# Optimization experiments

Measured on AMD Instinct MI355X. Metric: run time of the kernel, lower is better.

Reference implementation:

```python
import jax, jax.numpy as jnp
import numpy as np

N = 100000      # nodes
E = 1600000     # edges (avg in-degree 16)
IN_DIM = 256
HID_DIM = 256
OUT_DIM = 32
K = 16          # propagation hops


def _xavier(key, fan_in, fan_out, gain=1.0):
    a = gain * (6.0 / (fan_in + fan_out)) ** 0.5
    return jax.random.uniform(key, (fan_in, fan_out), jnp.float32, -a, a)


def setup_inputs() -> dict:
    key = jax.random.key(0)
    ks = jax.random.split(key, 8)
    feats = jax.random.normal(ks[0], (N, IN_DIM), jnp.float32)
    relu_gain = 2.0 ** 0.5
    W1 = _xavier(ks[1], IN_DIM, HID_DIM, relu_gain)
    b1 = jnp.zeros((HID_DIM,), jnp.float32)
    W2 = _xavier(ks[2], HID_DIM, HID_DIM, relu_gain)
    b2 = jnp.zeros((HID_DIM,), jnp.float32)
    W3 = _xavier(ks[3], HID_DIM, OUT_DIM, 1.0)
    b3 = jnp.zeros((OUT_DIM,), jnp.float32)
    s = _xavier(ks[4], OUT_DIM, 1, 1.0)  # sigmoid gain = 1.0
    src = jax.random.randint(ks[5], (E,), 0, N, jnp.int32)
    dst = jax.random.randint(ks[6], (E,), 0, N, jnp.int32)
    return {"feats": feats, "W1": W1, "b1": b1, "W2": W2, "b2": b2,
            "W3": W3, "b3": b3, "s": s, "src": src, "dst": dst}


def reference(feats, W1, b1, W2, b2, W3, b3, s, src, dst):
    # MLP stack (dropout is identity at inference)
    x = jax.nn.relu(feats @ W1 + b1)
    x = jax.nn.relu(x @ W2 + b2)
    x = x @ W3 + b3  # [N, OUT_DIM]

    # symmetric degree normalization from in-degrees (count of dst)
    degs = jax.ops.segment_sum(jnp.ones((E,), jnp.float32), dst, num_segments=N)
    norm = jnp.where(degs > 0, degs ** -0.5, 0.0)[:, None]  # [N,1]

    # k-hop normalized SpMM propagation: h <- D^-1/2 A^T D^-1/2 h
    def step(h, _):
        msgs = (h * norm)[src]                                  # gather, [E,D]
        h2 = jax.ops.segment_sum(msgs, dst, num_segments=N) * norm
        return h2, h2

    _, hs = jax.lax.scan(step, x, None, length=K)  # [K, N, D]
    H = jnp.concatenate([x[None], hs], axis=0).transpose(1, 0, 2)  # [N, K+1, D]

    # sigmoid-gated attention pooling over hops
    S = jax.nn.sigmoid(jnp.einsum('nkd,d->nk', H, s[:, 0]))  # [N, K+1]
    out = jnp.einsum('nk,nkd->nd', S, H)                      # [N, D]
    return out
```

## Files before the change

### kernel.cpp

```cpp
#include <hip/hip_runtime.h>
#include <hip/hip_bf16.h>
#include <cstdint>

typedef short bf16x8 __attribute__((ext_vector_type(8)));
typedef float f32x4 __attribute__((ext_vector_type(4)));
typedef unsigned short u16x8 __attribute__((ext_vector_type(8)));

#define BSHIFT 8
#define NBMAX 512

__device__ __forceinline__ ushort f2bf(float x) {
  uint32_t u = __float_as_uint(x);
  u += 0x7FFFu + ((u >> 16) & 1u);
  return (ushort)(u >> 16);
}
__device__ __forceinline__ float bf2f(ushort b) {
  return __uint_as_float((uint32_t)b << 16);
}

__device__ __forceinline__ void gload16(const void* g, void* l) {
  __builtin_amdgcn_global_load_lds((const __attribute__((address_space(1))) uint32_t*)g,
                                   (__attribute__((address_space(3))) uint32_t*)l, 16, 0, 0);
}

__global__ __launch_bounds__(256) void k_f32_to_bf16(const float* __restrict__ in,
                                                     ushort* __restrict__ out, int n4) {
  int i = blockIdx.x * 256 + threadIdx.x;
  if (i >= n4) return;
  const float4 v = reinterpret_cast<const float4*>(in)[i];
  ushort4 o;
  o.x = f2bf(v.x); o.y = f2bf(v.y); o.z = f2bf(v.z); o.w = f2bf(v.w);
  reinterpret_cast<ushort4*>(out)[i] = o;
}

__global__ __launch_bounds__(256) void k_convT(const float* __restrict__ W,
                                               ushort* __restrict__ Bt, int K, int Nc) {
  int i = blockIdx.x * 256 + threadIdx.x;
  if (i >= K * Nc) return;
  int nn = i / K, kk = i - nn * K;
  Bt[i] = f2bf(W[kk * Nc + nn]);
}

__global__ __launch_bounds__(256) void k_gemm1(const ushort* __restrict__ A,
                                               const ushort* __restrict__ Bt,
                                               const float* __restrict__ bias,
                                               ushort* __restrict__ Cout, int M, int ldc) {
  constexpr int BM = 128, BK = 64, KTOT = 256;
  constexpr int WM = 64, WN = 64, MR = 4, NR = 4;
  __shared__ ushort lA[2][BM * BK];
  __shared__ ushort lB[2][BM * BK];
  const int tid = threadIdx.x;
  const int w = tid >> 6, lane = tid & 63;
  const int wr = w >> 1, wc = w & 1;
  const int bm = blockIdx.x * BM;
  const int bn = blockIdx.y * BM;
  f32x4 acc[MR][NR] = {};

  auto stage = [&](int buf, int ks) {
    #pragma unroll
    for (int c0 = 0; c0 < 4; ++c0) {
      int c = c0 * 256 + tid;
      int r = c >> 3, ch = c & 7;
      int sch = (ch ^ (r & 7)) << 3;
      gload16(A + (size_t)(bm + r) * KTOT + ks + sch, lA[buf] + c * 8);
      gload16(Bt + (size_t)(bn + r) * KTOT + ks + sch, lB[buf] + c * 8);
    }
  };

  stage(0, 0);
  __syncthreads();
  int cur = 0;
  for (int kst = 0; kst < 4; ++kst) {
    if (kst < 3) stage(cur ^ 1, (kst + 1) * BK);
    #pragma unroll
    for (int kk = 0; kk < 2; ++kk) {
      bf16x8 af[MR], bfr[NR];
      int kc = kk * 4 + (lane >> 4);
      #pragma unroll
      for (int m = 0; m < MR; ++m) {
        int r = wr * WM + m * 16 + (lane & 15);
        af[m] = *reinterpret_cast<const bf16x8*>(lA[cur] + r * BK + (kc ^ (r & 7)) * 8);
      }
      #pragma unroll
      for (int n = 0; n < NR; ++n) {
        int r = wc * WN + n * 16 + (lane & 15);
        bfr[n] = *reinterpret_cast<const bf16x8*>(lB[cur] + r * BK + (kc ^ (r & 7)) * 8);
      }
      #pragma unroll
      for (int m = 0; m < MR; ++m)
        #pragma unroll
        for (int n = 0; n < NR; ++n)
          acc[m][n] = __builtin_amdgcn_mfma_f32_16x16x32_bf16(af[m], bfr[n], acc[m][n], 0, 0, 0);
    }
    __syncthreads();
    cur ^= 1;
  }
  #pragma unroll
  for (int m = 0; m < MR; ++m) {
    #pragma unroll
    for (int n = 0; n < NR; ++n) {
      int col = bn + wc * WN + n * 16 + (lane & 15);
      float bv = bias[col];
      #pragma unroll
      for (int j = 0; j < 4; ++j) {
        int row = bm + wr * WM + m * 16 + (lane >> 4) * 4 + j;
        if (row < M) {
          float v = fmaxf(acc[m][n][j] + bv, 0.f);
          Cout[(size_t)row * ldc + col] = f2bf(v);
        }
      }
    }
  }
}

__global__ __launch_bounds__(256) void k_gemm23(const ushort* __restrict__ x1,
                                                const ushort* __restrict__ w2t,
                                                const float* __restrict__ b2,
                                                const ushort* __restrict__ w3t,
                                                const float* __restrict__ b3,
                                                const float* __restrict__ svec,
                                                const float* __restrict__ nrm,
                                                float* __restrict__ xout,
                                                ushort* __restrict__ hs0, int M) {
  constexpr int BM = 64, BK = 64, KTOT = 256;
  constexpr int MR = 4, NR = 4;
  __shared__ char smem[40960];
  ushort* lA = (ushort*)smem;
  ushort* lB = (ushort*)(smem + 8192);
  ushort* lh2 = (ushort*)smem;
  const int tid = threadIdx.x;
  const int wv = tid >> 6, lane = tid & 63;
  const int bm = blockIdx.x * BM;
  f32x4 acc[MR][NR] = {};

  for (int ks = 0; ks < KTOT; ks += BK) {
    #pragma unroll
    for (int c0 = 0; c0 < 2; ++c0) {
      int c = c0 * 256 + tid;
      int r = c >> 3, ch = c & 7;
      gload16(x1 + (size_t)(bm + r) * KTOT + ks + ((ch ^ (r & 7)) << 3), lA + c * 8);
    }
    #pragma unroll
    for (int c0 = 0; c0 < 8; ++c0) {
      int c = c0 * 256 + tid;
      int r = c >> 3, ch = c & 7;
      gload16(w2t + (size_t)r * KTOT + ks + ((ch ^ (r & 7)) << 3), lB + c * 8);
    }
    __syncthreads();
    #pragma unroll
    for (int kk = 0; kk < 2; ++kk) {
      bf16x8 af[MR], bfr[NR];
      int kc = kk * 4 + (lane >> 4);
      #pragma unroll
      for (int m = 0; m < MR; ++m) {
        int r = m * 16 + (lane & 15);
        af[m] = *reinterpret_cast<const bf16x8*>(lA + r * BK + (kc ^ (r & 7)) * 8);
      }
      #pragma unroll
      for (int n = 0; n < NR; ++n) {
        int r = wv * 64 + n * 16 + (lane & 15);
        bfr[n] = *reinterpret_cast<const bf16x8*>(lB + r * BK + (kc ^ (r & 7)) * 8);
      }
      #pragma unroll
      for (int m = 0; m < MR; ++m)
        #pragma unroll
        for (int n = 0; n < NR; ++n)
          acc[m][n] = __builtin_amdgcn_mfma_f32_16x16x32_bf16(af[m], bfr[n], acc[m][n], 0, 0, 0);
    }
    __syncthreads();
  }

  #pragma unroll
  for (int n = 0; n < NR; ++n) {
    int col = wv * 64 + n * 16 + (lane & 15);
    float bv = b2[col];
    #pragma unroll
    for (int m = 0; m < MR; ++m) {
      #pragma unroll
      for (int j = 0; j < 4; ++j) {
        int row = m * 16 + (lane >> 4) * 4 + j;
        float v = fmaxf(acc[m][n][j] + bv, 0.f);
        int ch = col >> 3;
        int within = col & 7;
        lh2[row * 256 + ((ch ^ (row & 7)) << 3) + within] = f2bf(v);
      }
    }
  }
  __syncthreads();

  f32x4 acc3[2] = {};
  #pragma unroll
  for (int ks3 = 0; ks3 < 8; ++ks3) {
    int row = wv * 16 + (lane & 15);
    int kc = ks3 * 4 + (lane >> 4);
    bf16x8 af = *reinterpret_cast<const bf16x8*>(lh2 + row * 256 + ((kc ^ (row & 7)) << 3));
    #pragma unroll
    for (int n = 0; n < 2; ++n) {
      int col = n * 16 + (lane & 15);
      bf16x8 bfr = *reinterpret_cast<const bf16x8*>(w3t + (size_t)col * KTOT + kc * 8);
      acc3[n] = __builtin_amdgcn_mfma_f32_16x16x32_bf16(af, bfr, acc3[n], 0, 0, 0);
    }
  }
  float bb0 = b3[(lane & 15)];
  float bb1 = b3[16 + (lane & 15)];
  float sv0 = svec[(lane & 15)];
  float sv1 = svec[16 + (lane & 15)];
  #pragma unroll
  for (int j = 0; j < 4; ++j) {
    float x0 = acc3[0][j] + bb0;
    float x1v = acc3[1][j] + bb1;
    float p = x0 * sv0 + x1v * sv1;
    #pragma unroll
    for (int msk = 1; msk <= 8; msk <<= 1) p += __shfl_xor(p, msk);
    float g = 1.f / (1.f + __expf(-p));
    int row = bm + wv * 16 + (lane >> 4) * 4 + j;
    if (row < M) {
      float nv = nrm[row];
      xout[(size_t)row * 32 + (lane & 15)] = g * x0;
      xout[(size_t)row * 32 + 16 + (lane & 15)] = g * x1v;
      hs0[(size_t)row * 32 + (lane & 15)] = f2bf(x0 * nv);
      hs0[(size_t)row * 32 + 16 + (lane & 15)] = f2bf(x1v * nv);
    }
  }
}

__global__ __launch_bounds__(256) void k_bucket_hist(const int* __restrict__ dst,
                                                     int* __restrict__ bhist, int E) {
  __shared__ int lh[NBMAX];
  const int t = threadIdx.x;
  const int base = blockIdx.x * 4096;
  for (int i = t; i < NBMAX; i += 256) lh[i] = 0;
  __syncthreads();
  #pragma unroll
  for (int j = 0; j < 16; ++j) {
    int e = base + t + j * 256;
    if (e < E) atomicAdd(&lh[dst[e] >> BSHIFT], 1);
  }
  __syncthreads();
  for (int i = t; i < NBMAX; i += 256)
    if (lh[i]) atomicAdd(&bhist[i], lh[i]);
}

__global__ __launch_bounds__(256) void k_bucket_scan(const int* __restrict__ bhist,
                                                     int* __restrict__ bbase) {
  __shared__ int sh[256];
  int t = threadIdx.x;
  int v0 = bhist[2 * t], v1 = bhist[2 * t + 1];
  int s = v0 + v1;
  sh[t] = s;
  __syncthreads();
  for (int off = 1; off < 256; off <<= 1) {
    int x = (t >= off) ? sh[t - off] : 0;
    __syncthreads();
    sh[t] += x;
    __syncthreads();
  }
  int pre = sh[t] - s;
  bbase[2 * t] = pre;
  bbase[2 * t + 1] = pre + v0;
  if (t == 255) bbase[NBMAX] = sh[255];
}

__global__ __launch_bounds__(256) void k_bucket_scatter(const int* __restrict__ src,
                                                        const int* __restrict__ dst,
                                                        const int* __restrict__ bbase,
                                                        int* __restrict__ gfill,
                                                        int* __restrict__ tmp,
                                                        int E, int nbuck) {
  __shared__ int lhist[NBMAX];
  __shared__ int lbase[NBMAX];
  const int t = threadIdx.x;
  const int base = blockIdx.x * 4096;
  for (int i = t; i < NBMAX; i += 256) lhist[i] = 0;
  __syncthreads();
  int myd[16];
  #pragma unroll
  for (int j = 0; j < 16; ++j) {
    int e = base + t + j * 256;
    myd[j] = (e < E) ? dst[e] : -1;
    if (myd[j] >= 0) atomicAdd(&lhist[myd[j] >> BSHIFT], 1);
  }
  __syncthreads();
  for (int i = t; i < nbuck; i += 256) {
    int c = lhist[i];
    lbase[i] = (c > 0) ? atomicAdd(&gfill[i], c) : 0;
    lhist[i] = 0;
  }
  __syncthreads();
  #pragma unroll
  for (int j = 0; j < 16; ++j) {
    int e = base + t + j * 256;
    if (myd[j] >= 0) {
      int b = myd[j] >> BSHIFT;
      int r = atomicAdd(&lhist[b], 1);
      int pos = bbase[b] + lbase[b] + r;
      tmp[pos] = src[e] | ((myd[j] & 255) << 17);
    }
  }
}

__global__ __launch_bounds__(256) void k_bucket_sort(const int* __restrict__ tmp,
                                                     const int* __restrict__ bbase,
                                                     int* __restrict__ rp,
                                                     float* __restrict__ nrm,
                                                     float* __restrict__ invdeg,
                                                     float* __restrict__ sdeg,
                                                     int* __restrict__ ss,
                                                     int Nn, int E) {
  __shared__ int lcnt[256];
  __shared__ int sh[256];
  __shared__ int lpre[256];
  __shared__ int lfill[256];
  const int t = threadIdx.x;
  const int b = blockIdx.x;
  const int node0 = b << BSHIFT;
  const int seg0 = bbase[b], seg1 = bbase[b + 1];
  lcnt[t] = 0;
  lfill[t] = 0;
  __syncthreads();
  for (int i = seg0 + t; i < seg1; i += 256)
    atomicAdd(&lcnt[tmp[i] >> 17], 1);
  __syncthreads();
  int c = lcnt[t];
  sh[t] = c;
  __syncthreads();
  for (int off = 1; off < 256; off <<= 1) {
    int x = (t >= off) ? sh[t - off] : 0;
    __syncthreads();
    sh[t] += x;
    __syncthreads();
  }
  int pre = seg0 + sh[t] - c;
  lpre[t] = pre;
  int node = node0 + t;
  if (node < Nn) {
    rp[node] = pre;
    nrm[node] = (c > 0) ? rsqrtf((float)c) : 0.f;
    invdeg[node] = (c > 0) ? (1.f / (float)c) : 0.f;
    sdeg[node] = sqrtf((float)c);
  }
  if (b == 0 && t == 0) rp[Nn] = E;
  __syncthreads();
  for (int i = seg0 + t; i < seg1; i += 256) {
    int p = tmp[i];
    int n = p >> 17;
    int r = atomicAdd(&lfill[n], 1);
    ss[lpre[n] + r] = p & 0x1FFFF;
  }
}

__global__ __launch_bounds__(256) void k_prop(const ushort* __restrict__ hs_in,
                                              ushort* __restrict__ hs_out,
                                              const int* __restrict__ rp,
                                              const int* __restrict__ ss,
                                              const float* __restrict__ invdeg, int Nn) {
  const int wave = threadIdx.x >> 6;
  const int lane = threadIdx.x & 63;
  const int e4 = lane >> 4;
  const int d16 = lane & 15;
  const int v = blockIdx.x * 4 + wave;
  if (v >= Nn) return;
  const int beg = rp[v], end = rp[v + 1];
  float a0 = 0.f, a1 = 0.f;
  if (beg < end) {
    const int last = end - 1;
    const int i0 = beg + e4, i1 = i0 + 4, i2 = i0 + 8, i3 = i0 + 12;
    const int u0 = ss[min(i0, last)];
    const int u1 = ss[min(i1, last)];
    const int u2 = ss[min(i2, last)];
    const int u3 = ss[min(i3, last)];
    const uint r0 = *reinterpret_cast<const uint*>(hs_in + (size_t)u0 * 32 + d16 * 2);
    const uint r1 = *reinterpret_cast<const uint*>(hs_in + (size_t)u1 * 32 + d16 * 2);
    const uint r2 = *reinterpret_cast<const uint*>(hs_in + (size_t)u2 * 32 + d16 * 2);
    const uint r3 = *reinterpret_cast<const uint*>(hs_in + (size_t)u3 * 32 + d16 * 2);
    const float m0 = (i0 < end) ? 1.f : 0.f;
    const float m1 = (i1 < end) ? 1.f : 0.f;
    const float m2 = (i2 < end) ? 1.f : 0.f;
    const float m3 = (i3 < end) ? 1.f : 0.f;
    a0 = m0 * bf2f((ushort)r0) + m1 * bf2f((ushort)r1)
       + m2 * bf2f((ushort)r2) + m3 * bf2f((ushort)r3);
    a1 = m0 * bf2f((ushort)(r0 >> 16)) + m1 * bf2f((ushort)(r1 >> 16))
       + m2 * bf2f((ushort)(r2 >> 16)) + m3 * bf2f((ushort)(r3 >> 16));
    for (int i = i0 + 16; i < end; i += 4) {
      int u = ss[i];
      uint r = *reinterpret_cast<const uint*>(hs_in + (size_t)u * 32 + d16 * 2);
      a0 += bf2f((ushort)r);
      a1 += bf2f((ushort)(r >> 16));
    }
  }
  a0 += __shfl_xor(a0, 16); a1 += __shfl_xor(a1, 16);
  a0 += __shfl_xor(a0, 32); a1 += __shfl_xor(a1, 32);
  if (e4 == 0) {
    const float idv = invdeg[v];
    uint o = (uint)f2bf(a0 * idv) | ((uint)f2bf(a1 * idv) << 16);
    *reinterpret_cast<uint*>(hs_out + (size_t)v * 32 + d16 * 2) = o;
  }
}

__global__ __launch_bounds__(256) void k_pool(const ushort* __restrict__ hsF,
                                              const ushort* __restrict__ hsX,
                                              const ushort* __restrict__ hs16,
                                              const float* __restrict__ sdeg,
                                              const float* __restrict__ svec,
                                              float* __restrict__ xout, int Nn) {
  const int t = blockIdx.x * 256 + threadIdx.x;
  const int v = t >> 2;
  const int d4 = t & 3;
  if (v >= Nn) return;
  const float sd = sdeg[v];
  const float4 svA = *reinterpret_cast<const float4*>(svec + d4 * 8);
  const float4 svB = *reinterpret_cast<const float4*>(svec + d4 * 8 + 4);
  const size_t seg = (size_t)Nn * 32;
  const size_t off = (size_t)v * 32 + d4 * 8;
  float o0 = 0, o1 = 0, o2 = 0, o3 = 0, o4 = 0, o5 = 0, o6 = 0, o7 = 0;
  #pragma unroll
  for (int k = 1; k <= 16; ++k) {
    const ushort* hp = (k < 8) ? (hsF + (size_t)k * seg)
                     : (k < 16) ? (hsX + (size_t)(k - 8) * seg)
                                : hs16;
    u16x8 h = *reinterpret_cast<const u16x8*>(hp + off);
    float h0 = bf2f(h[0]) * sd, h1 = bf2f(h[1]) * sd, h2 = bf2f(h[2]) * sd, h3 = bf2f(h[3]) * sd;
    float h4 = bf2f(h[4]) * sd, h5 = bf2f(h[5]) * sd, h6 = bf2f(h[6]) * sd, h7 = bf2f(h[7]) * sd;
    float p = h0 * svA.x + h1 * svA.y + h2 * svA.z + h3 * svA.w
            + h4 * svB.x + h5 * svB.y + h6 * svB.z + h7 * svB.w;
    p += __shfl_xor(p, 1);
    p += __shfl_xor(p, 2);
    const float g = 1.f / (1.f + __expf(-p));
    o0 += g * h0; o1 += g * h1; o2 += g * h2; o3 += g * h3;
    o4 += g * h4; o5 += g * h5; o6 += g * h6; o7 += g * h7;
  }
  float4* oa = reinterpret_cast<float4*>(xout + off);
  float4 q0 = oa[0], q1 = oa[1];
  q0.x += o0; q0.y += o1; q0.z += o2; q0.w += o3;
  q1.x += o4; q1.y += o5; q1.z += o6; q1.w += o7;
  oa[0] = q0; oa[1] = q1;
}

extern "C" void kernel_launch(void* const* d_in, const int* in_sizes, int n_in,
                              void* d_out, int out_size, void* d_ws, size_t ws_size,
                              hipStream_t stream) {
  const float* feats = (const float*)d_in[0];
  const float* W1 = (const float*)d_in[1];
  const float* b1 = (const float*)d_in[2];
  const float* W2 = (const float*)d_in[3];
  const float* b2 = (const float*)d_in[4];
  const float* W3 = (const float*)d_in[5];
  const float* b3 = (const float*)d_in[6];
  const float* svec = (const float*)d_in[7];
  const int* src = (const int*)d_in[8];
  const int* dst = (const int*)d_in[9];

  const int DIN = 256, DH = 256, DOUT = 32, KHOP = 16;
  const int N = in_sizes[0] / DIN;
  const int E = in_sizes[8];
  const int nbuck = (N + (1 << BSHIFT) - 1) >> BSHIFT;

  char* w = (char*)d_ws;
  auto alloc = [&](size_t bytes) {
    char* p = w;
    w += (bytes + 255) & ~(size_t)255;
    return p;
  };
  ushort* featsb = (ushort*)alloc((size_t)N * DIN * 2);
  ushort* x1b = (ushort*)alloc((size_t)N * DH * 2);
  ushort* w1t = (ushort*)alloc((size_t)DIN * DH * 2);
  ushort* w2t = (ushort*)alloc((size_t)DH * DH * 2);
  ushort* w3t = (ushort*)alloc((size_t)DH * DOUT * 2);
  ushort* hs16 = (ushort*)alloc((size_t)N * DOUT * 2);
  float* nrm = (float*)alloc((size_t)N * 4);
  float* invdeg = (float*)alloc((size_t)N * 4);
  float* sdeg = (float*)alloc((size_t)N * 4);
  int* rp  = (int*)alloc((size_t)(N + 1) * 4);
  int* bhist = (int*)alloc((size_t)NBMAX * 4);
  int* bbase = (int*)alloc((size_t)(NBMAX + 1) * 4);
  int* gfill = (int*)alloc((size_t)NBMAX * 4);
  int* ss  = (int*)alloc((size_t)E * 4);
  int* tmp = (int*)alloc((size_t)E * 4);
  float* xout = (float*)d_out;

  const size_t seg = (size_t)N * DOUT;
  auto hsptr = [&](int k) -> ushort* {
    if (k < 8) return featsb + (size_t)k * seg;
    if (k < 16) return x1b + (size_t)(k - 8) * seg;
    return hs16;
  };

  k_f32_to_bf16<<<dim3((N * DIN / 4 + 255) / 256), 256, 0, stream>>>(feats, featsb, N * DIN / 4);
  k_convT<<<dim3((DIN * DH + 255) / 256), 256, 0, stream>>>(W1, w1t, DIN, DH);
  k_convT<<<dim3((DH * DH + 255) / 256), 256, 0, stream>>>(W2, w2t, DH, DH);
  k_convT<<<dim3((DH * DOUT + 255) / 256), 256, 0, stream>>>(W3, w3t, DH, DOUT);

  (void)hipMemsetAsync(bhist, 0, (size_t)NBMAX * 4, stream);
  (void)hipMemsetAsync(gfill, 0, (size_t)NBMAX * 4, stream);
  int nchunk = (E + 4095) / 4096;
  k_bucket_hist<<<dim3(nchunk), 256, 0, stream>>>(dst, bhist, E);
  k_bucket_scan<<<dim3(1), 256, 0, stream>>>(bhist, bbase);
  k_bucket_scatter<<<dim3(nchunk), 256, 0, stream>>>(src, dst, bbase, gfill, tmp, E, nbuck);
  k_bucket_sort<<<dim3(nbuck), 256, 0, stream>>>(tmp, bbase, rp, nrm, invdeg, sdeg, ss, N, E);

  dim3 g1((N + 127) / 128, DH / 128);
  k_gemm1<<<g1, 256, 0, stream>>>(featsb, w1t, b1, x1b, N, DH);
  k_gemm23<<<dim3((N + 63) / 64), 256, 0, stream>>>(x1b, w2t, b2, w3t, b3, svec, nrm, xout,
                                                    hsptr(0), N);

  for (int h = 0; h < KHOP; ++h) {
    k_prop<<<dim3((N + 3) / 4), 256, 0, stream>>>(hsptr(h), hsptr(h + 1), rp, ss, invdeg, N);
  }
  k_pool<<<dim3((N * 4 + 255) / 256), 256, 0, stream>>>(hsptr(0), hsptr(8), hs16, sdeg, svec,
                                                        xout, N);
}
```

Before: 748.5 us.

## Split hop features into two 16-column halves and propagate each half separately

Changes the per-hop bf16 feature layout from row-major [N,32] to two planar [N,16] halves, and runs the 16-hop propagation twice, once per half. The working set per propagation pass is halved (about 3.2MB instead of 6.4MB), so the random gathers are more likely to hit in cache. In exchange it launches twice as many prop kernels, each 32-byte gather uses a smaller transaction, and the pool kernel reads the new split layout.

After: 1.128 ms. 1.51x slower.

```diff
diff --git a/kernel.cpp b/kernel.cpp
--- a/kernel.cpp
+++ b/kernel.cpp
@@ -218,8 +218,8 @@
       float nv = nrm[row];
       xout[(size_t)row * 32 + (lane & 15)] = g * x0;
       xout[(size_t)row * 32 + 16 + (lane & 15)] = g * x1v;
-      hs0[(size_t)row * 32 + (lane & 15)] = f2bf(x0 * nv);
-      hs0[(size_t)row * 32 + 16 + (lane & 15)] = f2bf(x1v * nv);
+      hs0[(size_t)row * 16 + (lane & 15)] = f2bf(x0 * nv);
+      hs0[(size_t)M * 16 + (size_t)row * 16 + (lane & 15)] = f2bf(x1v * nv);
     }
   }
 }
@@ -349,51 +349,46 @@
   }
 }
 
-__global__ __launch_bounds__(256) void k_prop(const ushort* __restrict__ hs_in,
-                                              ushort* __restrict__ hs_out,
-                                              const int* __restrict__ rp,
-                                              const int* __restrict__ ss,
-                                              const float* __restrict__ invdeg, int Nn) {
+__global__ __launch_bounds__(256) void k_prop_half(const ushort* __restrict__ hs_in,
+                                                   ushort* __restrict__ hs_out,
+                                                   const int* __restrict__ rp,
+                                                   const int* __restrict__ ss,
+                                                   const float* __restrict__ invdeg,
+                                                   int Nn, int hbase) {
   const int wave = threadIdx.x >> 6;
   const int lane = threadIdx.x & 63;
-  const int e4 = lane >> 4;
-  const int d16 = lane & 15;
+  const int e8 = lane >> 3;
+  const int d8 = lane & 7;
   const int v = blockIdx.x * 4 + wave;
   if (v >= Nn) return;
   const int beg = rp[v], end = rp[v + 1];
+  const ushort* hin = hs_in + hbase;
   float a0 = 0.f, a1 = 0.f;
   if (beg < end) {
     const int last = end - 1;
-    const int i0 = beg + e4, i1 = i0 + 4, i2 = i0 + 8, i3 = i0 + 12;
+    const int i0 = beg + e8, i1 = i0 + 8;
     const int u0 = ss[min(i0, last)];
     const int u1 = ss[min(i1, last)];
-    const int u2 = ss[min(i2, last)];
-    const int u3 = ss[min(i3, last)];
-    const uint r0 = *reinterpret_cast<const uint*>(hs_in + (size_t)u0 * 32 + d16 * 2);
-    const uint r1 = *reinterpret_cast<const uint*>(hs_in + (size_t)u1 * 32 + d16 * 2);
-    const uint r2 = *reinterpret_cast<const uint*>(hs_in + (size_t)u2 * 32 + d16 * 2);
-    const uint r3 = *reinterpret_cast<const uint*>(hs_in + (size_t)u3 * 32 + d16 * 2);
+    const uint r0 = *reinterpret_cast<const uint*>(hin + (size_t)u0 * 16 + d8 * 2);
+    const uint r1 = *reinterpret_cast<const uint*>(hin + (size_t)u1 * 16 + d8 * 2);
     const float m0 = (i0 < end) ? 1.f : 0.f;
     const float m1 = (i1 < end) ? 1.f : 0.f;
-    const float m2 = (i2 < end) ? 1.f : 0.f;
-    const float m3 = (i3 < end) ? 1.f : 0.f;
-    a0 = m0 * bf2f((ushort)r0) + m1 * bf2f((ushort)r1)
-       + m2 * bf2f((ushort)r2) + m3 * bf2f((ushort)r3);
-    a1 = m0 * bf2f((ushort)(r0 >> 16)) + m1 * bf2f((ushort)(r1 >> 16))
-       + m2 * bf2f((ushort)(r2 >> 16)) + m3 * bf2f((ushort)(r3 >> 16));
-    for (int i = i0 + 16; i < end; i += 4) {
+    a0 = m0 * bf2f((ushort)r0) + m1 * bf2f((ushort)r1);
+    a1 = m0 * bf2f((ushort)(r0 >> 16)) + m1 * bf2f((ushort)(r1 >> 16));
+    for (int i = i1 + 8; i < end; i += 8) {
       int u = ss[i];
-      uint r = *reinterpret_cast<const uint*>(hs_in + (size_t)u * 32 + d16 * 2);
+      uint r = *reinterpret_cast<const uint*>(hin + (size_t)u * 16 + d8 * 2);
       a0 += bf2f((ushort)r);
       a1 += bf2f((ushort)(r >> 16));
     }
   }
+  a0 += __shfl_xor(a0, 8);  a1 += __shfl_xor(a1, 8);
   a0 += __shfl_xor(a0, 16); a1 += __shfl_xor(a1, 16);
   a0 += __shfl_xor(a0, 32); a1 += __shfl_xor(a1, 32);
-  if (e4 == 0) {
+  if (e8 == 0) {
     const float idv = invdeg[v];
     uint o = (uint)f2bf(a0 * idv) | ((uint)f2bf(a1 * idv) << 16);
-    *reinterpret_cast<uint*>(hs_out + (size_t)v * 32 + d16 * 2) = o;
+    *reinterpret_cast<uint*>(hs_out + hbase + (size_t)v * 16 + d8 * 2) = o;
   }
 }
 
@@ -411,7 +406,8 @@
   const float4 svA = *reinterpret_cast<const float4*>(svec + d4 * 8);
   const float4 svB = *reinterpret_cast<const float4*>(svec + d4 * 8 + 4);
   const size_t seg = (size_t)Nn * 32;
-  const size_t off = (size_t)v * 32 + d4 * 8;
+  const int half = d4 >> 1, sub = d4 & 1;
+  const size_t off = (size_t)half * Nn * 16 + (size_t)v * 16 + sub * 8;
   float o0 = 0, o1 = 0, o2 = 0, o3 = 0, o4 = 0, o5 = 0, o6 = 0, o7 = 0;
   #pragma unroll
   for (int k = 1; k <= 16; ++k) {
@@ -429,7 +425,7 @@
     o0 += g * h0; o1 += g * h1; o2 += g * h2; o3 += g * h3;
     o4 += g * h4; o5 += g * h5; o6 += g * h6; o7 += g * h7;
   }
-  float4* oa = reinterpret_cast<float4*>(xout + off);
+  float4* oa = reinterpret_cast<float4*>(xout + (size_t)v * 32 + d4 * 8);
   float4 q0 = oa[0], q1 = oa[1];
   q0.x += o0; q0.y += o1; q0.z += o2; q0.w += o3;
   q1.x += o4; q1.y += o5; q1.z += o6; q1.w += o7;
@@ -503,8 +499,12 @@
   k_gemm23<<<dim3((N + 63) / 64), 256, 0, stream>>>(x1b, w2t, b2, w3t, b3, svec, nrm, xout,
                                                     hsptr(0), N);
 
-  for (int h = 0; h < KHOP; ++h) {
-    k_prop<<<dim3((N + 3) / 4), 256, 0, stream>>>(hsptr(h), hsptr(h + 1), rp, ss, invdeg, N);
+  for (int half = 0; half < 2; ++half) {
+    const int hbase = half * N * 16;
+    for (int h = 0; h < KHOP; ++h) {
+      k_prop_half<<<dim3((N + 3) / 4), 256, 0, stream>>>(hsptr(h), hsptr(h + 1), rp, ss,
+                                                         invdeg, N, hbase);
+    }
   }
   k_pool<<<dim3((N * 4 + 255) / 256), 256, 0, stream>>>(hsptr(0), hsptr(8), hs16, sdeg, svec,
                                                         xout, N);
```

## Widen gemm1 tile to full 256 output columns and drop double buffering

Applied to the files above, without the earlier changes.

The first MLP GEMM now computes a 128x256 tile per block, covering the whole hidden width. Each A row tile is therefore loaded once instead of twice across a second grid column. Per-warp accumulators double to 4x8 MFMA tiles. The LDS double buffer is replaced by a single buffer with sync-load-compute. This keeps LDS use similar but removes the overlap of loads with MFMA, and the larger accumulator set raises register pressure and may lower occupancy.

Result: slower. 768.7 us (+2.7%).

```diff
diff --git a/kernel.cpp b/kernel.cpp
--- a/kernel.cpp
+++ b/kernel.cpp
@@ -45,33 +45,32 @@
                                                const ushort* __restrict__ Bt,
                                                const float* __restrict__ bias,
                                                ushort* __restrict__ Cout, int M, int ldc) {
-  constexpr int BM = 128, BK = 64, KTOT = 256;
-  constexpr int WM = 64, WN = 64, MR = 4, NR = 4;
-  __shared__ ushort lA[2][BM * BK];
-  __shared__ ushort lB[2][BM * BK];
+  constexpr int BM = 128, BN = 256, BK = 64, KTOT = 256;
+  constexpr int WM = 64, WN = 128, MR = 4, NR = 8;
+  __shared__ ushort lA[BM * BK];
+  __shared__ ushort lB[BN * BK];
   const int tid = threadIdx.x;
   const int w = tid >> 6, lane = tid & 63;
   const int wr = w >> 1, wc = w & 1;
   const int bm = blockIdx.x * BM;
-  const int bn = blockIdx.y * BM;
   f32x4 acc[MR][NR] = {};
 
-  auto stage = [&](int buf, int ks) {
+  for (int ks = 0; ks < KTOT; ks += BK) {
     #pragma unroll
     for (int c0 = 0; c0 < 4; ++c0) {
       int c = c0 * 256 + tid;
       int r = c >> 3, ch = c & 7;
       int sch = (ch ^ (r & 7)) << 3;
-      gload16(A + (size_t)(bm + r) * KTOT + ks + sch, lA[buf] + c * 8);
-      gload16(Bt + (size_t)(bn + r) * KTOT + ks + sch, lB[buf] + c * 8);
-    }
-  };
-
-  stage(0, 0);
-  __syncthreads();
-  int cur = 0;
-  for (int kst = 0; kst < 4; ++kst) {
-    if (kst < 3) stage(cur ^ 1, (kst + 1) * BK);
+      gload16(A + (size_t)(bm + r) * KTOT + ks + sch, lA + c * 8);
+    }
+    #pragma unroll
+    for (int c0 = 0; c0 < 8; ++c0) {
+      int c = c0 * 256 + tid;
+      int r = c >> 3, ch = c & 7;
+      int sch = (ch ^ (r & 7)) << 3;
+      gload16(Bt + (size_t)r * KTOT + ks + sch, lB + c * 8);
+    }
+    __syncthreads();
     #pragma unroll
     for (int kk = 0; kk < 2; ++kk) {
       bf16x8 af[MR], bfr[NR];
@@ -79,12 +78,12 @@
       #pragma unroll
       for (int m = 0; m < MR; ++m) {
         int r = wr * WM + m * 16 + (lane & 15);
-        af[m] = *reinterpret_cast<const bf16x8*>(lA[cur] + r * BK + (kc ^ (r & 7)) * 8);
+        af[m] = *reinterpret_cast<const bf16x8*>(lA + r * BK + (kc ^ (r & 7)) * 8);
       }
       #pragma unroll
       for (int n = 0; n < NR; ++n) {
         int r = wc * WN + n * 16 + (lane & 15);
-        bfr[n] = *reinterpret_cast<const bf16x8*>(lB[cur] + r * BK + (kc ^ (r & 7)) * 8);
+        bfr[n] = *reinterpret_cast<const bf16x8*>(lB + r * BK + (kc ^ (r & 7)) * 8);
       }
       #pragma unroll
       for (int m = 0; m < MR; ++m)
@@ -93,13 +92,12 @@
           acc[m][n] = __builtin_amdgcn_mfma_f32_16x16x32_bf16(af[m], bfr[n], acc[m][n], 0, 0, 0);
     }
     __syncthreads();
-    cur ^= 1;
   }
   #pragma unroll
   for (int m = 0; m < MR; ++m) {
     #pragma unroll
     for (int n = 0; n < NR; ++n) {
-      int col = bn + wc * WN + n * 16 + (lane & 15);
+      int col = wc * WN + n * 16 + (lane & 15);
       float bv = bias[col];
       #pragma unroll
       for (int j = 0; j < 4; ++j) {
@@ -498,8 +496,7 @@
   k_bucket_scatter<<<dim3(nchunk), 256, 0, stream>>>(src, dst, bbase, gfill, tmp, E, nbuck);
   k_bucket_sort<<<dim3(nbuck), 256, 0, stream>>>(tmp, bbase, rp, nrm, invdeg, sdeg, ss, N, E);
 
-  dim3 g1((N + 127) / 128, DH / 128);
-  k_gemm1<<<g1, 256, 0, stream>>>(featsb, w1t, b1, x1b, N, DH);
+  k_gemm1<<<dim3((N + 127) / 128), 256, 0, stream>>>(featsb, w1t, b1, x1b, N, DH);
   k_gemm23<<<dim3((N + 63) / 64), 256, 0, stream>>>(x1b, w2t, b2, w3t, b3, svec, nrm, xout,
                                                     hsptr(0), N);
 
```
